# Kernel tuning notes

Hardware: AMD Instinct MI355X
Metric: run time of the kernel (lower is better)

The kernel has to match this reference:

```python
import jax, jax.numpy as jnp
import numpy as np
import math

NBITS = (1, 2, 4, 8)
S, B, D, H, F = 1024, 8, 1024, 16, 4096
HD = D // H


def _quant(w, nbit):
    """Symmetric uniform weight quantization to `nbit` bits with STE."""
    if nbit == 1:
        q = jnp.sign(w) * jnp.mean(jnp.abs(w))
    else:
        qmax = float(2 ** (nbit - 1) - 1)
        scale = jnp.max(jnp.abs(w)) / qmax
        q = jnp.clip(jnp.round(w / scale), -qmax - 1.0, qmax) * scale
    # straight-through estimator: forward uses q, backward flows through w
    return w + jax.lax.stop_gradient(q - w)


def _layernorm(x, g, b, eps=1e-5):
    m = jnp.mean(x, axis=-1, keepdims=True)
    v = jnp.var(x, axis=-1, keepdims=True)
    return (x - m) * jax.lax.rsqrt(v + eps) * g + b


def _quant_attn(src, w_in, b_in, w_out, b_out, nbit):
    # src: [S,B,D]; w_in: [3D,D]; w_out: [D,D]
    w_in_q = _quant(w_in, nbit)
    w_out_q = _quant(w_out, nbit)
    qkv = jnp.einsum('sbd,ed->sbe', src, w_in_q) + b_in  # [S,B,3D]
    q, k, v = jnp.split(qkv, 3, axis=-1)
    q = q.reshape(S, B, H, HD)
    k = k.reshape(S, B, H, HD)
    v = v.reshape(S, B, H, HD)
    scores = jnp.einsum('sbhd,tbhd->bhst', q, k) * (1.0 / math.sqrt(HD))
    p = jax.nn.softmax(scores, axis=-1)  # [B,H,S,S]
    o = jnp.einsum('bhst,tbhd->sbhd', p, v).reshape(S, B, D)
    return jnp.einsum('sbd,ed->sbe', o, w_out_q) + b_out


def setup_inputs() -> dict:
    key = jax.random.key(0)
    ks = jax.random.split(key, 12)
    sc = 0.02
    return {
        'src': jax.random.normal(ks[0], (S, B, D), jnp.float32),
        'alpha': jax.random.normal(ks[1], (3, 4), jnp.float32),
        'in_proj_w': jax.random.normal(ks[2], (4, 3 * D, D), jnp.float32) * sc,
        'in_proj_b': jnp.zeros((4, 3 * D), jnp.float32),
        'out_proj_w': jax.random.normal(ks[3], (4, D, D), jnp.float32) * sc,
        'out_proj_b': jnp.zeros((4, D), jnp.float32),
        'w1': jax.random.normal(ks[4], (4, F, D), jnp.float32) * sc,
        'b1': jnp.zeros((4, F), jnp.float32),
        'w2': jax.random.normal(ks[5], (4, D, F), jnp.float32) * sc,
        'b2': jnp.zeros((4, D), jnp.float32),
        'g1': jnp.ones((D,), jnp.float32),
        'be1': jnp.zeros((D,), jnp.float32),
        'g2': jnp.ones((D,), jnp.float32),
        'be2': jnp.zeros((D,), jnp.float32),
    }


def reference(src, alpha, in_proj_w, in_proj_b, out_proj_w, out_proj_b,
              w1, b1, w2, b2, g1, be1, g2, be2):
    probs = jax.nn.softmax(alpha, axis=-1)  # [3,4]
    # softmax-weighted mixture of multi-bitwidth attention branches
    src2 = jnp.zeros_like(src)
    for i, nbit in enumerate(NBITS):
        src2 = src2 + probs[0, i] * _quant_attn(
            src, in_proj_w[i], in_proj_b[i], out_proj_w[i], out_proj_b[i], nbit)
    x = _layernorm(src + src2, g1, be1)
    # mixture of quantized linear1 branches, then GELU
    h = jnp.zeros((S, B, F), src.dtype)
    for i, nbit in enumerate(NBITS):
        h = h + probs[1, i] * (jnp.einsum('sbd,fd->sbf', x, _quant(w1[i], nbit)) + b1[i])
    h = jax.nn.gelu(h, approximate=False)
    # mixture of quantized linear2 branches
    y = jnp.zeros_like(x)
    for i, nbit in enumerate(NBITS):
        y = y + probs[2, i] * (jnp.einsum('sbf,df->sbd', h, _quant(w2[i], nbit)) + b2[i])
    return _layernorm(x + y, g2, be2)
```

## Files before the change

### kernel.cpp

```cpp
#include <hip/hip_runtime.h>
#include <hip/hip_bf16.h>

typedef __attribute__((ext_vector_type(8))) unsigned short u16x8;
typedef __attribute__((ext_vector_type(4))) unsigned short u16x4;
typedef __attribute__((ext_vector_type(4))) int            i32x4;
typedef __attribute__((ext_vector_type(8))) __bf16         bf16x8;
typedef __attribute__((ext_vector_type(4))) float          f32x4;

#define SS 1024
#define BB 8
#define DD 1024
#define HH 16
#define HDD 64
#define FF 4096
#define MM 8192

#define GL16(g, l) __builtin_amdgcn_global_load_lds( \
    (__attribute__((address_space(1))) const void*)(g), \
    (__attribute__((address_space(3))) void*)(l), 16, 0, 0)

__device__ __forceinline__ float bf2f(unsigned short u) {
    return __uint_as_float(((unsigned int)u) << 16);
}
__device__ __forceinline__ unsigned short f2bf(float f) {
    return __builtin_bit_cast(unsigned short, (__bf16)f);
}
__device__ __forceinline__ float quantv(float w, float som, float qm) {
    if (qm == 0.f) {
        float sgn = (w > 0.f) ? 1.f : ((w < 0.f) ? -1.f : 0.f);
        return sgn * som;
    }
    if (som == 0.f) return 0.f;
    float q = rintf(w / som);
    q = fminf(fmaxf(q, -qm - 1.f), qm);
    return q * som;
}

__global__ __launch_bounds__(256) void k_stats(const float* __restrict__ w_in, const float* __restrict__ w_out,
                                               const float* __restrict__ w1, const float* __restrict__ w2,
                                               const float* __restrict__ src,
                                               float* __restrict__ pmax, float* __restrict__ psum) {
    const int t = blockIdx.y, blk = blockIdx.x, tid = threadIdx.x;
    const float* base; int n;
    if (t < 4)       { base = w_in  + (size_t)t * 3145728;     n = 3145728; }
    else if (t < 8)  { base = w_out + (size_t)(t-4) * 1048576; n = 1048576; }
    else if (t < 12) { base = w1    + (size_t)(t-8) * 4194304; n = 4194304; }
    else if (t < 16) { base = w2    + (size_t)(t-12) * 4194304; n = 4194304; }
    else             { base = src;                             n = 8388608; }
    const int n4 = n >> 2;
    float vmax = 0.f, vsum = 0.f;
    for (int i = blk * 256 + tid; i < n4; i += 65536) {
        float4 v = reinterpret_cast<const float4*>(base)[i];
        float a0 = fabsf(v.x), a1 = fabsf(v.y), a2 = fabsf(v.z), a3 = fabsf(v.w);
        vmax = fmaxf(vmax, fmaxf(fmaxf(a0, a1), fmaxf(a2, a3)));
        vsum += (a0 + a1) + (a2 + a3);
    }
#pragma unroll
    for (int m = 1; m < 64; m <<= 1) { vmax = fmaxf(vmax, __shfl_xor(vmax, m, 64)); vsum += __shfl_xor(vsum, m, 64); }
    __shared__ float sm[4], su[4];
    const int wave = tid >> 6, lane = tid & 63;
    if (lane == 0) { sm[wave] = vmax; su[wave] = vsum; }
    __syncthreads();
    if (tid == 0) {
        pmax[t * 256 + blk] = fmaxf(fmaxf(sm[0], sm[1]), fmaxf(sm[2], sm[3]));
        psum[t * 256 + blk] = (su[0] + su[1]) + (su[2] + su[3]);
    }
}

__global__ __launch_bounds__(256) void k_params(const float* __restrict__ pmax, const float* __restrict__ psum,
                                                const float* __restrict__ alpha, float* __restrict__ P) {
    __shared__ float rm[256], rs[256];
    const int tid = threadIdx.x;
    for (int t = 0; t < 17; ++t) {
        rm[tid] = pmax[t * 256 + tid];
        rs[tid] = psum[t * 256 + tid];
        __syncthreads();
        for (int s = 128; s > 0; s >>= 1) {
            if (tid < s) { rm[tid] = fmaxf(rm[tid], rm[tid + s]); rs[tid] += rs[tid + s]; }
            __syncthreads();
        }
        if (tid == 0) {
            if (t == 16) {
                P[50] = rm[0] * (1.f / 127.f);
            } else {
                const int nbits[4] = {1, 2, 4, 8};
                const int nb = nbits[t & 3];
                float nsize = (t < 4) ? 3145728.f : ((t < 8) ? 1048576.f : 4194304.f);
                if (nb == 1) { P[16 + 2*t] = rs[0] / nsize; P[17 + 2*t] = 0.f; }
                else { float qm = (float)((1 << (nb - 1)) - 1); P[16 + 2*t] = rm[0] / qm; P[17 + 2*t] = qm; }
            }
        }
        __syncthreads();
    }
    if (tid < 3) {
        float a[4], mx = -1e30f;
#pragma unroll
        for (int i = 0; i < 4; ++i) { a[i] = alpha[tid * 4 + i]; mx = fmaxf(mx, a[i]); }
        float e[4], ssum = 0.f;
#pragma unroll
        for (int i = 0; i < 4; ++i) { e[i] = expf(a[i] - mx); ssum += e[i]; }
#pragma unroll
        for (int i = 0; i < 4; ++i) P[tid * 4 + i] = e[i] / ssum;
    }
}

__global__ __launch_bounds__(256) void k_rmax(const float* __restrict__ part, int n, float* __restrict__ out) {
    const int tid = threadIdx.x;
    float m = 0.f;
    for (int i = tid; i < n; i += 256) m = fmaxf(m, part[i]);
#pragma unroll
    for (int s = 1; s < 64; s <<= 1) m = fmaxf(m, __shfl_xor(m, s, 64));
    __shared__ float sm[4];
    const int wave = tid >> 6, lane = tid & 63;
    if (lane == 0) sm[wave] = m;
    __syncthreads();
    if (tid == 0) *out = fmaxf(fmaxf(sm[0], sm[1]), fmaxf(sm[2], sm[3]));
}

__global__ __launch_bounds__(256) void k_quant8(const float* __restrict__ w, signed char* __restrict__ out,
                                                const float* __restrict__ P, int per_tensor, int tbase, int ntot) {
    int i = blockIdx.x * 256 + threadIdx.x;
    if (i >= ntot) return;
    int t = tbase + i / per_tensor;
    float som = P[16 + 2*t], qm = P[17 + 2*t];
    float v;
    float x = w[i];
    if (qm == 0.f)      v = (x > 0.f) ? 1.f : ((x < 0.f) ? -1.f : 0.f);
    else if (som == 0.f) v = 0.f;
    else                v = fminf(fmaxf(rintf(x / som), -qm - 1.f), qm);
    out[i] = (signed char)(int)v;
}

__global__ __launch_bounds__(256) void k_si8(const float* __restrict__ in, signed char* __restrict__ out,
                                             const float* __restrict__ P, int n4) {
    int i = blockIdx.x * 256 + threadIdx.x;
    if (i >= n4) return;
    const float sa = P[50];
    const float inv = (sa > 0.f) ? 1.f / sa : 0.f;
    float4 v = reinterpret_cast<const float4*>(in)[i];
    char4 o;
    o.x = (signed char)(int)fminf(fmaxf(rintf(v.x * inv), -127.f), 127.f);
    o.y = (signed char)(int)fminf(fmaxf(rintf(v.y * inv), -127.f), 127.f);
    o.z = (signed char)(int)fminf(fmaxf(rintf(v.z * inv), -127.f), 127.f);
    o.w = (signed char)(int)fminf(fmaxf(rintf(v.w * inv), -127.f), 127.f);
    reinterpret_cast<char4*>(out)[i] = o;
}

template <int NE, int MODE>
__global__ __launch_bounds__(256) void k_mixq8(const float* __restrict__ w, signed char* __restrict__ out,
                                               float* __restrict__ sB, const float* __restrict__ P,
                                               int tbase, int prow, size_t sz) {
    const int row = blockIdx.x, tid = threadIdx.x;
    const int L = NE * 256;
    float v[NE];
    float lm = 0.f;
#pragma unroll
    for (int j = 0; j < NE; ++j) {
        int k = j * 256 + tid;
        float acc;
        if (MODE == 0) {
            acc = 0.f;
#pragma unroll
            for (int br = 0; br < 4; ++br) {
                int t = tbase + br;
                acc += P[prow * 4 + br] * quantv(w[(size_t)br * sz + (size_t)row * L + k], P[16 + 2*t], P[17 + 2*t]);
            }
        } else {
            int i = k >> 10, e = k & 1023;
            int t = tbase + i;
            acc = P[i] * quantv(w[(size_t)i * sz + (size_t)row * 1024 + e], P[16 + 2*t], P[17 + 2*t]);
        }
        v[j] = acc;
        lm = fmaxf(lm, fabsf(acc));
    }
#pragma unroll
    for (int m = 1; m < 64; m <<= 1) lm = fmaxf(lm, __shfl_xor(lm, m, 64));
    __shared__ float sm[4];
    const int wave = tid >> 6, lane = tid & 63;
    if (lane == 0) sm[wave] = lm;
    __syncthreads();
    lm = fmaxf(fmaxf(sm[0], sm[1]), fmaxf(sm[2], sm[3]));
    if (tid == 0) sB[row] = lm * (1.f / 127.f);
    const float inv = (lm > 0.f) ? 127.f / lm : 0.f;
#pragma unroll
    for (int j = 0; j < NE; ++j)
        out[(size_t)row * L + j * 256 + tid] =
            (signed char)(int)fminf(fmaxf(rintf(v[j] * inv), -127.f), 127.f);
}

__global__ __launch_bounds__(256) void k_mixb(const float* __restrict__ b, float* __restrict__ out,
                                              const float* __restrict__ P, int prow, int n) {
    int i = blockIdx.x * 256 + threadIdx.x;
    if (i >= n) return;
    float acc = 0.f;
#pragma unroll
    for (int br = 0; br < 4; ++br) acc += P[prow * 4 + br] * b[(size_t)br * n + i];
    out[i] = acc;
}

__global__ __launch_bounds__(256) void k_q8(const unsigned short* __restrict__ in, signed char* __restrict__ out,
                                            const float* __restrict__ amax, int n8) {
    int i = blockIdx.x * 256 + threadIdx.x;
    if (i >= n8) return;
    const float am = *amax;
    const float inv = (am > 0.f) ? 127.f / am : 0.f;
    u16x8 v = reinterpret_cast<const u16x8*>(in)[i];
    union { signed char c[8]; unsigned long long u; } r;
#pragma unroll
    for (int e = 0; e < 8; ++e) {
        float f = bf2f(v[e]) * inv;
        r.c[e] = (signed char)(int)fminf(fmaxf(rintf(f), -127.f), 127.f);
    }
    reinterpret_cast<unsigned long long*>(out)[i] = r.u;
}

__global__ __launch_bounds__(256) void k_gemm_i8(const signed char* __restrict__ A,
                                                 const signed char* __restrict__ Bw,
                                                 unsigned short* __restrict__ C,
                                                 const float* __restrict__ bias,
                                                 const float* __restrict__ P, int tIdx,
                                                 int M, int N, int K, int XM, int XN) {
    const int gx = gridDim.x, gy = gridDim.y;
    const int flat = blockIdx.x + gx * blockIdx.y;
    const int xcd = flat & 7, r = flat >> 3;
    const int nloc = gx / XN, mloc = gy / XM;
    const int cm = xcd / XN, cn = xcd - cm * XN;
    const int by = cm * mloc + r / nloc;
    const int bx = cn * nloc + (r - (r / nloc) * nloc);

    __shared__ signed char As[2][128 * 128];
    __shared__ signed char Bs[2][128 * 128];
    const int tid = threadIdx.x;
    const int m0 = by * 128, n0 = bx * 128;
    const int lane = tid & 63, wave = tid >> 6;
    const int wr = wave >> 1, wc = wave & 1;
    const int lr = lane & 15, lg = lane >> 4;
    const int rsub = lane >> 3;
    const int csub = ((lane & 7) ^ rsub) * 16;
    const size_t aoff = (size_t)(m0 + rsub) * K + csub;
    const size_t boff = (size_t)(n0 + rsub) * K + csub;

    i32x4 acc[4][4];
#pragma unroll
    for (int m = 0; m < 4; ++m)
#pragma unroll
        for (int n = 0; n < 4; ++n) acc[m][n] = (i32x4){0, 0, 0, 0};

    auto stage = [&](int buf, int k0) {
#pragma unroll
        for (int it = 0; it < 4; ++it) {
            const int g = it * 4 + wave;
            GL16(A + aoff + (size_t)g * 8 * K + k0, &As[buf][g * 1024]);
            GL16(Bw + boff + (size_t)g * 8 * K + k0, &Bs[buf][g * 1024]);
        }
    };
    auto compute = [&](int buf) {
#pragma unroll
        for (int kh = 0; kh < 2; ++kh) {
            i32x4 af[4], bfr[4];
#pragma unroll
            for (int m = 0; m < 4; ++m) {
                int row = wr * 64 + m * 16 + lr;
                int cidx = (kh * 4 + lg) ^ (lr & 7);
                af[m] = *reinterpret_cast<const i32x4*>(&As[buf][row * 128 + cidx * 16]);
            }
#pragma unroll
            for (int n = 0; n < 4; ++n) {
                int row = wc * 64 + n * 16 + lr;
                int cidx = (kh * 4 + lg) ^ (lr & 7);
                bfr[n] = *reinterpret_cast<const i32x4*>(&Bs[buf][row * 128 + cidx * 16]);
            }
#pragma unroll
            for (int m = 0; m < 4; ++m)
#pragma unroll
                for (int n = 0; n < 4; ++n)
                    acc[m][n] = __builtin_amdgcn_mfma_i32_16x16x64_i8(
                        af[m], bfr[n], acc[m][n], 0, 0, 0);
        }
    };

    stage(0, 0);
    __syncthreads();
    int cur = 0;
    for (int k0 = 128; k0 < K; k0 += 128) {
        stage(cur ^ 1, k0);
        compute(cur);
        __syncthreads();
        cur ^= 1;
    }
    compute(cur);

    const float sab = P[50] * P[16 + 2 * tIdx];
#pragma unroll
    for (int n = 0; n < 4; ++n) {
        const int col = n0 + wc * 64 + n * 16 + lr;
        const float bv = bias[col];
#pragma unroll
        for (int m = 0; m < 4; ++m) {
#pragma unroll
            for (int j = 0; j < 4; ++j) {
                const int row = m0 + wr * 64 + m * 16 + lg * 4 + j;
                float v = (float)acc[m][n][j] * sab + bv;
                C[(size_t)row * N + col] = f2bf(v);
            }
        }
    }
}

__device__ __forceinline__ void store_out(float* C, size_t idx, float v) { C[idx] = v; }
__device__ __forceinline__ void store_out(unsigned short* C, size_t idx, float v) { C[idx] = f2bf(v); }

template <typename OutT, bool GELU>
__global__ __launch_bounds__(256) void k_gemm_i8s(const signed char* __restrict__ A,
                                                  const signed char* __restrict__ Bw,
                                                  OutT* __restrict__ C,
                                                  const float* __restrict__ bias,
                                                  const float* __restrict__ sB,
                                                  const float* __restrict__ aAm,
                                                  float* __restrict__ oPart,
                                                  int M, int N, int K, int XM, int XN) {
    const int gx = gridDim.x, gy = gridDim.y;
    const int flat = blockIdx.x + gx * blockIdx.y;
    const int xcd = flat & 7, r = flat >> 3;
    const int nloc = gx / XN, mloc = gy / XM;
    const int cm = xcd / XN, cn = xcd - cm * XN;
    const int by = cm * mloc + r / nloc;
    const int bx = cn * nloc + (r - (r / nloc) * nloc);

    __shared__ signed char As[2][128 * 128];
    __shared__ signed char Bs[2][128 * 128];
    __shared__ float smx[4];
    const int tid = threadIdx.x;
    const int m0 = by * 128, n0 = bx * 128;
    const int lane = tid & 63, wave = tid >> 6;
    const int wr = wave >> 1, wc = wave & 1;
    const int lr = lane & 15, lg = lane >> 4;
    const int rsub = lane >> 3;
    const int csub = ((lane & 7) ^ rsub) * 16;
    const size_t aoff = (size_t)(m0 + rsub) * K + csub;
    const size_t boff = (size_t)(n0 + rsub) * K + csub;

    i32x4 acc[4][4];
#pragma unroll
    for (int m = 0; m < 4; ++m)
#pragma unroll
        for (int n = 0; n < 4; ++n) acc[m][n] = (i32x4){0, 0, 0, 0};

    auto stage = [&](int buf, int k0) {
#pragma unroll
        for (int it = 0; it < 4; ++it) {
            const int g = it * 4 + wave;
            GL16(A + aoff + (size_t)g * 8 * K + k0, &As[buf][g * 1024]);
            GL16(Bw + boff + (size_t)g * 8 * K + k0, &Bs[buf][g * 1024]);
        }
    };
    auto compute = [&](int buf) {
#pragma unroll
        for (int kh = 0; kh < 2; ++kh) {
            i32x4 af[4], bfr[4];
#pragma unroll
            for (int m = 0; m < 4; ++m) {
                int row = wr * 64 + m * 16 + lr;
                int cidx = (kh * 4 + lg) ^ (lr & 7);
                af[m] = *reinterpret_cast<const i32x4*>(&As[buf][row * 128 + cidx * 16]);
            }
#pragma unroll
            for (int n = 0; n < 4; ++n) {
                int row = wc * 64 + n * 16 + lr;
                int cidx = (kh * 4 + lg) ^ (lr & 7);
                bfr[n] = *reinterpret_cast<const i32x4*>(&Bs[buf][row * 128 + cidx * 16]);
            }
#pragma unroll
            for (int m = 0; m < 4; ++m)
#pragma unroll
                for (int n = 0; n < 4; ++n)
                    acc[m][n] = __builtin_amdgcn_mfma_i32_16x16x64_i8(
                        af[m], bfr[n], acc[m][n], 0, 0, 0);
        }
    };

    stage(0, 0);
    __syncthreads();
    int cur = 0;
    for (int k0 = 128; k0 < K; k0 += 128) {
        stage(cur ^ 1, k0);
        compute(cur);
        __syncthreads();
        cur ^= 1;
    }
    compute(cur);

    const float sA = (*aAm) * (1.f / 127.f);
    float lm = 0.f;
#pragma unroll
    for (int n = 0; n < 4; ++n) {
        const int col = n0 + wc * 64 + n * 16 + lr;
        const float sc = sA * sB[col];
        const float bv = bias ? bias[col] : 0.f;
#pragma unroll
        for (int m = 0; m < 4; ++m) {
#pragma unroll
            for (int j = 0; j < 4; ++j) {
                const int row = m0 + wr * 64 + m * 16 + lg * 4 + j;
                float v = (float)acc[m][n][j] * sc + bv;
                if (GELU) v = 0.5f * v * (1.f + erff(v * 0.70710678118654752f));
                store_out(C, (size_t)row * N + col, v);
                if (oPart) lm = fmaxf(lm, fabsf(v));
            }
        }
    }
    if (oPart) {
#pragma unroll
        for (int m = 1; m < 64; m <<= 1) lm = fmaxf(lm, __shfl_xor(lm, m, 64));
        if (lane == 0) smx[wave] = lm;
        __syncthreads();
        if (tid == 0) oPart[flat] = fmaxf(fmaxf(smx[0], smx[1]), fmaxf(smx[2], smx[3]));
    }
}

__global__ __launch_bounds__(256) void k_fmfma(const unsigned short* __restrict__ qkvb, int qstride,
                                               unsigned short* __restrict__ outb, int ostride,
                                               float* __restrict__ oPart) {
    __shared__ unsigned short Ks[64 * 64];
    __shared__ unsigned short Vt[64 * 64];
    __shared__ unsigned short Pl[4 * 16 * 72];
    __shared__ float smx[4];
    const int tid = threadIdx.x;
    const int lane = tid & 63, wave = tid >> 6;
    const int lr = lane & 15, lg = lane >> 4;
    const int f = blockIdx.x;
    const int bh = (f & 7) * 16 + (f >> 7);
    const int s0 = ((f >> 3) & 15) * 64;
    const int b = bh >> 4, hh = bh & 15;
    const int hb = hh * 64;

    u16x8 qf[2];
    {
        const size_t qb = (size_t)((s0 + wave * 16 + lr) * 8 + b) * qstride + hb;
#pragma unroll
        for (int ks = 0; ks < 2; ++ks)
            qf[ks] = *reinterpret_cast<const u16x8*>(qkvb + qb + ks * 32 + lg * 8);
    }
    const int rsub = lane >> 3;
    const int csub = ((lane & 7) ^ rsub) * 8;
    const unsigned short* kS = qkvb + (size_t)(rsub * 8 + b) * qstride + 1024 + hb + csub;

    float m_old = -1e30f, l_run = 0.f;
    f32x4 oacc[4];
#pragma unroll
    for (int n = 0; n < 4; ++n) oacc[n] = (f32x4){0.f, 0.f, 0.f, 0.f};
    unsigned short* myP = Pl + wave * (16 * 72);

    for (int kt = 0; kt < 16; ++kt) {
        __syncthreads();
#pragma unroll
        for (int it = 0; it < 2; ++it) {
            const int g = it * 4 + wave;
            GL16(kS + (size_t)((kt * 64 + g * 8) * 8) * qstride, &Ks[g * 512]);
        }
#pragma unroll
        for (int it = 0; it < 2; ++it) {
            int c = tid + it * 256;
            int row = c >> 3, ch = c & 7;
            const size_t gb = (size_t)((kt * 64 + row) * 8 + b) * qstride + hb + ch * 8;
            u16x8 vv = *reinterpret_cast<const u16x8*>(qkvb + gb + 2048);
            const int vbase = ((row >> 3) ^ ch) * 8 + (row & 7);
#pragma unroll
            for (int e = 0; e < 8; ++e) Vt[(ch * 8 + e) * 64 + (vbase ^ (e * 8))] = vv[e];
        }
        __syncthreads();
        f32x4 sacc[4];
#pragma unroll
        for (int n = 0; n < 4; ++n) sacc[n] = (f32x4){0.f, 0.f, 0.f, 0.f};
#pragma unroll
        for (int ks = 0; ks < 2; ++ks) {
#pragma unroll
            for (int n = 0; n < 4; ++n) {
                int row = n * 16 + lr;
                int cidx = (ks * 4 + lg) ^ (lr & 7);
                u16x8 kf = *reinterpret_cast<const u16x8*>(&Ks[row * 64 + cidx * 8]);
                sacc[n] = __builtin_amdgcn_mfma_f32_16x16x32_bf16(
                    __builtin_bit_cast(bf16x8, kf), __builtin_bit_cast(bf16x8, qf[ks]),
                    sacc[n], 0, 0, 0);
            }
        }
        float pmax = -1e30f;
#pragma unroll
        for (int n = 0; n < 4; ++n)
#pragma unroll
            for (int j = 0; j < 4; ++j) { sacc[n][j] *= 0.125f; pmax = fmaxf(pmax, sacc[n][j]); }
        pmax = fmaxf(pmax, __shfl_xor(pmax, 16, 64));
        pmax = fmaxf(pmax, __shfl_xor(pmax, 32, 64));
        const float m_new = fmaxf(m_old, pmax);
        const float corr = __expf(m_old - m_new);
        float pv[16];
        float psum = 0.f;
#pragma unroll
        for (int n = 0; n < 4; ++n)
#pragma unroll
            for (int j = 0; j < 4; ++j) { float e = __expf(sacc[n][j] - m_new); pv[n * 4 + j] = e; psum += e; }
        psum += __shfl_xor(psum, 16, 64);
        psum += __shfl_xor(psum, 32, 64);
        l_run = l_run * corr + psum;
        m_old = m_new;
#pragma unroll
        for (int n = 0; n < 4; ++n)
#pragma unroll
            for (int t2 = 0; t2 < 2; ++t2) {
                int key = n * 16 + lg * 4 + t2 * 2;
                unsigned int pk =
                    (unsigned int)__builtin_bit_cast(unsigned short, (__bf16)pv[n * 4 + t2 * 2]) |
                    ((unsigned int)__builtin_bit_cast(unsigned short, (__bf16)pv[n * 4 + t2 * 2 + 1]) << 16);
                *reinterpret_cast<unsigned int*>(&myP[lr * 72 + key]) = pk;
            }
#pragma unroll
        for (int j = 0; j < 4; ++j) {
            float cj = __shfl(corr, lg * 4 + j, 64);
#pragma unroll
            for (int n = 0; n < 4; ++n) oacc[n][j] *= cj;
        }
#pragma unroll
        for (int ks = 0; ks < 2; ++ks) {
            u16x8 pa = *reinterpret_cast<const u16x8*>(&myP[lr * 72 + ks * 32 + lg * 8]);
#pragma unroll
            for (int n = 0; n < 4; ++n) {
                int d = n * 16 + lr;
                int kcs = ((ks * 4 + lg) ^ (d >> 3)) ^ (d & 7);
                u16x8 vf = *reinterpret_cast<const u16x8*>(&Vt[d * 64 + kcs * 8]);
                oacc[n] = __builtin_amdgcn_mfma_f32_16x16x32_bf16(
                    __builtin_bit_cast(bf16x8, pa), __builtin_bit_cast(bf16x8, vf),
                    oacc[n], 0, 0, 0);
            }
        }
    }
    const float linv = 1.f / l_run;
    float lm = 0.f;
#pragma unroll
    for (int j = 0; j < 4; ++j) {
        float lj = __shfl(linv, lg * 4 + j, 64);
        const size_t rowb = (size_t)((s0 + wave * 16 + lg * 4 + j) * 8 + b) * ostride + hb;
#pragma unroll
        for (int n = 0; n < 4; ++n) {
            float v = oacc[n][j] * lj;
            outb[rowb + n * 16 + lr] = f2bf(v);
            lm = fmaxf(lm, fabsf(v));
        }
    }
#pragma unroll
    for (int m = 1; m < 64; m <<= 1) lm = fmaxf(lm, __shfl_xor(lm, m, 64));
    if (lane == 0) smx[wave] = lm;
    __syncthreads();
    if (tid == 0) oPart[f] = fmaxf(fmaxf(smx[0], smx[1]), fmaxf(smx[2], smx[3]));
}

__global__ __launch_bounds__(256) void k_ln(const float* __restrict__ xf, const unsigned short* __restrict__ xb,
                                            const float* __restrict__ r,
                                            const float* __restrict__ g, const float* __restrict__ be,
                                            float* __restrict__ outf, unsigned short* __restrict__ outb,
                                            float* __restrict__ oPart) {
    const int row = blockIdx.x, tid = threadIdx.x;
    const size_t base = (size_t)row * 1024 + tid * 4;
    float x0, x1, x2, x3;
    if (xf) {
        float4 xv = *reinterpret_cast<const float4*>(xf + base);
        x0 = xv.x; x1 = xv.y; x2 = xv.z; x3 = xv.w;
    } else {
        u16x4 xv = *reinterpret_cast<const u16x4*>(xb + base);
        x0 = bf2f(xv[0]); x1 = bf2f(xv[1]); x2 = bf2f(xv[2]); x3 = bf2f(xv[3]);
    }
    float4 rv = *reinterpret_cast<const float4*>(r + base);
    float t0 = x0 + rv.x, t1 = x1 + rv.y, t2 = x2 + rv.z, t3 = x3 + rv.w;
    float s = t0 + t1 + t2 + t3;
    float ss = t0 * t0 + t1 * t1 + t2 * t2 + t3 * t3;
#pragma unroll
    for (int m = 1; m < 64; m <<= 1) { s += __shfl_xor(s, m, 64); ss += __shfl_xor(ss, m, 64); }
    __shared__ float red[8];
    __shared__ float smx[4];
    const int wave = tid >> 6, lane = tid & 63;
    if (lane == 0) { red[wave] = s; red[4 + wave] = ss; }
    __syncthreads();
    s = red[0] + red[1] + red[2] + red[3];
    ss = red[4] + red[5] + red[6] + red[7];
    const float mean = s * (1.f / 1024.f);
    const float var = ss * (1.f / 1024.f) - mean * mean;
    const float rstd = rsqrtf(var + 1e-5f);
    float4 gv = *reinterpret_cast<const float4*>(g + tid * 4);
    float4 bv = *reinterpret_cast<const float4*>(be + tid * 4);
    float o0 = (t0 - mean) * rstd * gv.x + bv.x;
    float o1 = (t1 - mean) * rstd * gv.y + bv.y;
    float o2 = (t2 - mean) * rstd * gv.z + bv.z;
    float o3 = (t3 - mean) * rstd * gv.w + bv.w;
    if (outf) {
        float4 ov = {o0, o1, o2, o3};
        *reinterpret_cast<float4*>(outf + base) = ov;
    }
    if (outb) {
        u16x4 q; q[0] = f2bf(o0); q[1] = f2bf(o1); q[2] = f2bf(o2); q[3] = f2bf(o3);
        *reinterpret_cast<u16x4*>(outb + base) = q;
    }
    if (oPart) {
        float lm = fmaxf(fmaxf(fabsf(o0), fabsf(o1)), fmaxf(fabsf(o2), fabsf(o3)));
#pragma unroll
        for (int m = 1; m < 64; m <<= 1) lm = fmaxf(lm, __shfl_xor(lm, m, 64));
        if (lane == 0) smx[wave] = lm;
        __syncthreads();
        if (tid == 0) oPart[row] = fmaxf(fmaxf(smx[0], smx[1]), fmaxf(smx[2], smx[3]));
    }
}

extern "C" void kernel_launch(void* const* d_in, const int* in_sizes, int n_in,
                              void* d_out, int out_size, void* d_ws, size_t ws_size,
                              hipStream_t stream) {
    const float* src   = (const float*)d_in[0];
    const float* alpha = (const float*)d_in[1];
    const float* w_in  = (const float*)d_in[2];
    const float* b_in  = (const float*)d_in[3];
    const float* w_out = (const float*)d_in[4];
    const float* b_out = (const float*)d_in[5];
    const float* w1    = (const float*)d_in[6];
    const float* b1    = (const float*)d_in[7];
    const float* w2    = (const float*)d_in[8];
    const float* b2    = (const float*)d_in[9];
    const float* g1    = (const float*)d_in[10];
    const float* be1   = (const float*)d_in[11];
    const float* g2    = (const float*)d_in[12];
    const float* be2   = (const float*)d_in[13];

    char* ws = (char*)d_ws;
    size_t off = 0;
    auto alloc = [&](size_t bytes) { size_t r = off; off += (bytes + 255) & ~(size_t)255; return r; };
    float* P              = (float*)(ws + alloc(1024));
    float* amaxv          = (float*)(ws + alloc(256));
    float* flashPart      = (float*)(ws + alloc(8192 * 4));
    float* lnPart         = (float*)(ws + alloc(8192 * 4));
    float* hPart          = (float*)(ws + alloc(2048 * 4));
    float* pmax           = (float*)(ws + alloc(17 * 256 * 4));
    float* psum           = (float*)(ws + alloc(17 * 256 * 4));
    signed char* WinQ8    = (signed char*)(ws + alloc((size_t)4 * 3072 * 1024));
    signed char* WoutC8   = (signed char*)(ws + alloc((size_t)1024 * 4096));
    float* sOut           = (float*)(ws + alloc(1024 * 4));
    signed char* W1m8     = (signed char*)(ws + alloc((size_t)4096 * 1024));
    float* s1             = (float*)(ws + alloc(4096 * 4));
    signed char* W2m8     = (signed char*)(ws + alloc((size_t)1024 * 4096));
    float* s2             = (float*)(ws + alloc(1024 * 4));
    float* b1m            = (float*)(ws + alloc(4096 * 4));
    float* b2m            = (float*)(ws + alloc(1024 * 4));
    float* bOm            = (float*)(ws + alloc(1024 * 4));
    signed char* Si8      = (signed char*)(ws + alloc((size_t)MM * 1024));
    unsigned short* Xbf   = (unsigned short*)(ws + alloc((size_t)MM * 1024 * 2));
    signed char* Xi8      = (signed char*)(ws + alloc((size_t)MM * 1024));
    unsigned short* attnC = (unsigned short*)(ws + alloc((size_t)MM * 4096 * 2));
    unsigned short* qkvB  = (unsigned short*)(ws + alloc((size_t)MM * 3072 * 2));
    signed char* attnC8   = (signed char*)qkvB;
    unsigned short* h     = attnC;
    signed char* h8       = (signed char*)qkvB;
    if (ws_size < off) return;

    float* outF = (float*)d_out;

    k_stats<<<dim3(256, 17), 256, 0, stream>>>(w_in, w_out, w1, w2, src, pmax, psum);
    k_params<<<1, 256, 0, stream>>>(pmax, psum, alpha, P);
    {
        int n = 4 * 3072 * 1024;
        k_quant8<<<(n + 255) / 256, 256, 0, stream>>>(w_in, WinQ8, P, 3072 * 1024, 0, n);
        k_mixq8<16, 1><<<1024, 256, 0, stream>>>(w_out, WoutC8, sOut, P, 4, 0, 1048576);
        k_mixq8<4, 0><<<4096, 256, 0, stream>>>(w1, W1m8, s1, P, 8, 1, 4194304);
        k_mixq8<16, 0><<<1024, 256, 0, stream>>>(w2, W2m8, s2, P, 12, 2, 4194304);
        k_mixb<<<(4096 + 255) / 256, 256, 0, stream>>>(b1, b1m, P, 1, 4096);
        k_mixb<<<(1024 + 255) / 256, 256, 0, stream>>>(b2, b2m, P, 2, 1024);
        k_mixb<<<(1024 + 255) / 256, 256, 0, stream>>>(b_out, bOm, P, 0, 1024);
        k_si8<<<(2097152 + 255) / 256, 256, 0, stream>>>(src, Si8, P, 2097152);
    }
    for (int i = 0; i < 4; ++i) {
        k_gemm_i8<<<dim3(24, 64), 256, 0, stream>>>(
            Si8, WinQ8 + (size_t)i * 3072 * 1024, qkvB, b_in + i * 3072, P, i, MM, 3072, 1024, 1, 8);
        k_fmfma<<<dim3(2048), 256, 0, stream>>>(qkvB, 3072, attnC + i * 1024, 4096,
                                                flashPart + i * 2048);
    }
    k_rmax<<<1, 256, 0, stream>>>(flashPart, 8192, amaxv + 0);
    k_q8<<<(4194304 + 255) / 256, 256, 0, stream>>>(attnC, attnC8, amaxv + 0, 4194304);
    k_gemm_i8s<float, false><<<dim3(8, 64), 256, 0, stream>>>(
        attnC8, WoutC8, outF, bOm, sOut, amaxv + 0, nullptr, MM, 1024, 4096, 4, 2);
    k_ln<<<MM, 256, 0, stream>>>(src, nullptr, outF, g1, be1, nullptr, Xbf, lnPart);
    k_rmax<<<1, 256, 0, stream>>>(lnPart, 8192, amaxv + 1);
    k_q8<<<(1048576 + 255) / 256, 256, 0, stream>>>(Xbf, Xi8, amaxv + 1, 1048576);
    k_gemm_i8s<unsigned short, true><<<dim3(32, 64), 256, 0, stream>>>(
        Xi8, W1m8, h, b1m, s1, amaxv + 1, hPart, MM, 4096, 1024, 1, 8);
    k_rmax<<<1, 256, 0, stream>>>(hPart, 2048, amaxv + 2);
    k_q8<<<(4194304 + 255) / 256, 256, 0, stream>>>(h, h8, amaxv + 2, 4194304);
    k_gemm_i8s<float, false><<<dim3(8, 64), 256, 0, stream>>>(
        h8, W2m8, outF, b2m, s2, amaxv + 2, nullptr, MM, 1024, 4096, 4, 2);
    k_ln<<<MM, 256, 0, stream>>>(nullptr, Xbf, outF, g2, be2, outF, nullptr, nullptr);
}
```

Baseline: 934.8 us.

## Double-buffer K/V tiles and process two query subtiles per wave in flash attention

The flash-attention kernel now uses 512-thread blocks covering 256 query rows each, and each wave handles two 16-row query subtiles. This reuses every staged K/V tile across more queries. K and V tiles are double-buffered so the next tile's loads are issued before computing on the current one, leaving one barrier per iteration. The row-sum reduction is deferred to the end. The grid shrinks to a quarter of its previous size, which may reduce parallelism, and LDS and register use rise.

```diff
diff --git a/kernel.cpp b/kernel.cpp
--- a/kernel.cpp
+++ b/kernel.cpp
@@ -418,139 +418,154 @@
     }
 }
 
-__global__ __launch_bounds__(256) void k_fmfma(const unsigned short* __restrict__ qkvb, int qstride,
+__global__ __launch_bounds__(512) void k_fmfma(const unsigned short* __restrict__ qkvb, int qstride,
                                                unsigned short* __restrict__ outb, int ostride,
                                                float* __restrict__ oPart) {
-    __shared__ unsigned short Ks[64 * 64];
-    __shared__ unsigned short Vt[64 * 64];
-    __shared__ unsigned short Pl[4 * 16 * 72];
-    __shared__ float smx[4];
+    __shared__ unsigned short Ks[2][4096];
+    __shared__ unsigned short Vt[2][4096];
+    __shared__ unsigned short Pl[8 * 16 * 72];
+    __shared__ float smx[8];
     const int tid = threadIdx.x;
     const int lane = tid & 63, wave = tid >> 6;
     const int lr = lane & 15, lg = lane >> 4;
     const int f = blockIdx.x;
-    const int bh = (f & 7) * 16 + (f >> 7);
-    const int s0 = ((f >> 3) & 15) * 64;
+    const int bh = (f & 7) * 16 + ((f >> 3) & 15);
+    const int s0 = (f >> 7) * 256;
     const int b = bh >> 4, hh = bh & 15;
     const int hb = hh * 64;
 
-    u16x8 qf[2];
-    {
-        const size_t qb = (size_t)((s0 + wave * 16 + lr) * 8 + b) * qstride + hb;
+    u16x8 qf[2][2];
+#pragma unroll
+    for (int qf2 = 0; qf2 < 2; ++qf2) {
+        const size_t qb = (size_t)((s0 + wave * 32 + qf2 * 16 + lr) * 8 + b) * qstride + hb;
 #pragma unroll
         for (int ks = 0; ks < 2; ++ks)
-            qf[ks] = *reinterpret_cast<const u16x8*>(qkvb + qb + ks * 32 + lg * 8);
+            qf[qf2][ks] = *reinterpret_cast<const u16x8*>(qkvb + qb + ks * 32 + lg * 8);
     }
     const int rsub = lane >> 3;
     const int csub = ((lane & 7) ^ rsub) * 8;
     const unsigned short* kS = qkvb + (size_t)(rsub * 8 + b) * qstride + 1024 + hb + csub;
 
-    float m_old = -1e30f, l_run = 0.f;
-    f32x4 oacc[4];
-#pragma unroll
-    for (int n = 0; n < 4; ++n) oacc[n] = (f32x4){0.f, 0.f, 0.f, 0.f};
+    float m_old[2] = {-1e30f, -1e30f};
+    float l_lane[2] = {0.f, 0.f};
+    f32x4 oacc[2][4];
+#pragma unroll
+    for (int qf2 = 0; qf2 < 2; ++qf2)
+#pragma unroll
+        for (int n = 0; n < 4; ++n) oacc[qf2][n] = (f32x4){0.f, 0.f, 0.f, 0.f};
     unsigned short* myP = Pl + wave * (16 * 72);
 
+    auto stage = [&](int buf, int kt) {
+        GL16(kS + (size_t)((kt * 64 + wave * 8) * 8) * qstride, &Ks[buf][wave * 512]);
+        const int row = tid >> 3, ch = tid & 7;
+        const size_t gb = (size_t)((kt * 64 + row) * 8 + b) * qstride + hb + ch * 8;
+        u16x8 vv = *reinterpret_cast<const u16x8*>(qkvb + gb + 2048);
+        const int vbase = ((row >> 3) ^ ch) * 8 + (row & 7);
+#pragma unroll
+        for (int e = 0; e < 8; ++e) Vt[buf][(ch * 8 + e) * 64 + (vbase ^ (e * 8))] = vv[e];
+    };
+
+    stage(0, 0);
+    __syncthreads();
+    int cur = 0;
     for (int kt = 0; kt < 16; ++kt) {
+        if (kt < 15) stage(cur ^ 1, kt + 1);
+#pragma unroll
+        for (int qf2 = 0; qf2 < 2; ++qf2) {
+            f32x4 sacc[4];
+#pragma unroll
+            for (int n = 0; n < 4; ++n) sacc[n] = (f32x4){0.f, 0.f, 0.f, 0.f};
+#pragma unroll
+            for (int ks = 0; ks < 2; ++ks) {
+#pragma unroll
+                for (int n = 0; n < 4; ++n) {
+                    int row = n * 16 + lr;
+                    int cidx = (ks * 4 + lg) ^ (lr & 7);
+                    u16x8 kf = *reinterpret_cast<const u16x8*>(&Ks[cur][row * 64 + cidx * 8]);
+                    sacc[n] = __builtin_amdgcn_mfma_f32_16x16x32_bf16(
+                        __builtin_bit_cast(bf16x8, kf), __builtin_bit_cast(bf16x8, qf[qf2][ks]),
+                        sacc[n], 0, 0, 0);
+                }
+            }
+            float pmax = -1e30f;
+#pragma unroll
+            for (int n = 0; n < 4; ++n)
+#pragma unroll
+                for (int j = 0; j < 4; ++j) { sacc[n][j] *= 0.125f; pmax = fmaxf(pmax, sacc[n][j]); }
+            pmax = fmaxf(pmax, __shfl_xor(pmax, 16, 64));
+            pmax = fmaxf(pmax, __shfl_xor(pmax, 32, 64));
+            const float m_new = fmaxf(m_old[qf2], pmax);
+            const float corr = __expf(m_old[qf2] - m_new);
+            float pv[16];
+            float psum = 0.f;
+#pragma unroll
+            for (int n = 0; n < 4; ++n)
+#pragma unroll
+                for (int j = 0; j < 4; ++j) { float e = __expf(sacc[n][j] - m_new); pv[n * 4 + j] = e; psum += e; }
+            l_lane[qf2] = l_lane[qf2] * corr + psum;
+            m_old[qf2] = m_new;
+#pragma unroll
+            for (int n = 0; n < 4; ++n)
+#pragma unroll
+                for (int t2 = 0; t2 < 2; ++t2) {
+                    int key = n * 16 + lg * 4 + t2 * 2;
+                    unsigned int pk =
+                        (unsigned int)__builtin_bit_cast(unsigned short, (__bf16)pv[n * 4 + t2 * 2]) |
+                        ((unsigned int)__builtin_bit_cast(unsigned short, (__bf16)pv[n * 4 + t2 * 2 + 1]) << 16);
+                    *reinterpret_cast<unsigned int*>(&myP[lr * 72 + key]) = pk;
+                }
+#pragma unroll
+            for (int j = 0; j < 4; ++j) {
+                float cj = __shfl(corr, lg * 4 + j, 64);
+#pragma unroll
+                for (int n = 0; n < 4; ++n) oacc[qf2][n][j] *= cj;
+            }
+#pragma unroll
+            for (int ks = 0; ks < 2; ++ks) {
+                u16x8 pa = *reinterpret_cast<const u16x8*>(&myP[lr * 72 + ks * 32 + lg * 8]);
+#pragma unroll
+                for (int n = 0; n < 4; ++n) {
+                    int d = n * 16 + lr;
+                    int kcs = ((ks * 4 + lg) ^ (d >> 3)) ^ (d & 7);
+                    u16x8 vf = *reinterpret_cast<const u16x8*>(&Vt[cur][d * 64 + kcs * 8]);
+                    oacc[qf2][n] = __builtin_amdgcn_mfma_f32_16x16x32_bf16(
+                        __builtin_bit_cast(bf16x8, pa), __builtin_bit_cast(bf16x8, vf),
+                        oacc[qf2][n], 0, 0, 0);
+                }
+            }
+        }
         __syncthreads();
-#pragma unroll
-        for (int it = 0; it < 2; ++it) {
-            const int g = it * 4 + wave;
-            GL16(kS + (size_t)((kt * 64 + g * 8) * 8) * qstride, &Ks[g * 512]);
-        }
-#pragma unroll
-        for (int it = 0; it < 2; ++it) {
-            int c = tid + it * 256;
-            int row = c >> 3, ch = c & 7;
-            const size_t gb = (size_t)((kt * 64 + row) * 8 + b) * qstride + hb + ch * 8;
-            u16x8 vv = *reinterpret_cast<const u16x8*>(qkvb + gb + 2048);
-            const int vbase = ((row >> 3) ^ ch) * 8 + (row & 7);
-#pragma unroll
-            for (int e = 0; e < 8; ++e) Vt[(ch * 8 + e) * 64 + (vbase ^ (e * 8))] = vv[e];
-        }
-        __syncthreads();
-        f32x4 sacc[4];
-#pragma unroll
-        for (int n = 0; n < 4; ++n) sacc[n] = (f32x4){0.f, 0.f, 0.f, 0.f};
-#pragma unroll
-        for (int ks = 0; ks < 2; ++ks) {
+        cur ^= 1;
+    }
+    float lm = 0.f;
+#pragma unroll
+    for (int qf2 = 0; qf2 < 2; ++qf2) {
+        float lsum = l_lane[qf2];
+        lsum += __shfl_xor(lsum, 16, 64);
+        lsum += __shfl_xor(lsum, 32, 64);
+        const float linv = 1.f / lsum;
+#pragma unroll
+        for (int j = 0; j < 4; ++j) {
+            float lj = __shfl(linv, lg * 4 + j, 64);
+            const size_t rowb = (size_t)((s0 + wave * 32 + qf2 * 16 + lg * 4 + j) * 8 + b) * ostride + hb;
 #pragma unroll
             for (int n = 0; n < 4; ++n) {
-                int row = n * 16 + lr;
-                int cidx = (ks * 4 + lg) ^ (lr & 7);
-                u16x8 kf = *reinterpret_cast<const u16x8*>(&Ks[row * 64 + cidx * 8]);
-                sacc[n] = __builtin_amdgcn_mfma_f32_16x16x32_bf16(
-                    __builtin_bit_cast(bf16x8, kf), __builtin_bit_cast(bf16x8, qf[ks]),
-                    sacc[n], 0, 0, 0);
-            }
-        }
-        float pmax = -1e30f;
-#pragma unroll
-        for (int n = 0; n < 4; ++n)
-#pragma unroll
-            for (int j = 0; j < 4; ++j) { sacc[n][j] *= 0.125f; pmax = fmaxf(pmax, sacc[n][j]); }
-        pmax = fmaxf(pmax, __shfl_xor(pmax, 16, 64));
-        pmax = fmaxf(pmax, __shfl_xor(pmax, 32, 64));
-        const float m_new = fmaxf(m_old, pmax);
-        const float corr = __expf(m_old - m_new);
-        float pv[16];
-        float psum = 0.f;
-#pragma unroll
-        for (int n = 0; n < 4; ++n)
-#pragma unroll
-            for (int j = 0; j < 4; ++j) { float e = __expf(sacc[n][j] - m_new); pv[n * 4 + j] = e; psum += e; }
-        psum += __shfl_xor(psum, 16, 64);
-        psum += __shfl_xor(psum, 32, 64);
-        l_run = l_run * corr + psum;
-        m_old = m_new;
-#pragma unroll
-        for (int n = 0; n < 4; ++n)
-#pragma unroll
-            for (int t2 = 0; t2 < 2; ++t2) {
-                int key = n * 16 + lg * 4 + t2 * 2;
-                unsigned int pk =
-                    (unsigned int)__builtin_bit_cast(unsigned short, (__bf16)pv[n * 4 + t2 * 2]) |
-                    ((unsigned int)__builtin_bit_cast(unsigned short, (__bf16)pv[n * 4 + t2 * 2 + 1]) << 16);
-                *reinterpret_cast<unsigned int*>(&myP[lr * 72 + key]) = pk;
-            }
-#pragma unroll
-        for (int j = 0; j < 4; ++j) {
-            float cj = __shfl(corr, lg * 4 + j, 64);
-#pragma unroll
-            for (int n = 0; n < 4; ++n) oacc[n][j] *= cj;
-        }
-#pragma unroll
-        for (int ks = 0; ks < 2; ++ks) {
-            u16x8 pa = *reinterpret_cast<const u16x8*>(&myP[lr * 72 + ks * 32 + lg * 8]);
-#pragma unroll
-            for (int n = 0; n < 4; ++n) {
-                int d = n * 16 + lr;
-                int kcs = ((ks * 4 + lg) ^ (d >> 3)) ^ (d & 7);
-                u16x8 vf = *reinterpret_cast<const u16x8*>(&Vt[d * 64 + kcs * 8]);
-                oacc[n] = __builtin_amdgcn_mfma_f32_16x16x32_bf16(
-                    __builtin_bit_cast(bf16x8, pa), __builtin_bit_cast(bf16x8, vf),
-                    oacc[n], 0, 0, 0);
-            }
-        }
-    }
-    const float linv = 1.f / l_run;
-    float lm = 0.f;
-#pragma unroll
-    for (int j = 0; j < 4; ++j) {
-        float lj = __shfl(linv, lg * 4 + j, 64);
-        const size_t rowb = (size_t)((s0 + wave * 16 + lg * 4 + j) * 8 + b) * ostride + hb;
-#pragma unroll
-        for (int n = 0; n < 4; ++n) {
-            float v = oacc[n][j] * lj;
-            outb[rowb + n * 16 + lr] = f2bf(v);
-            lm = fmaxf(lm, fabsf(v));
+                float v = oacc[qf2][n][j] * lj;
+                outb[rowb + n * 16 + lr] = f2bf(v);
+                lm = fmaxf(lm, fabsf(v));
+            }
         }
     }
 #pragma unroll
     for (int m = 1; m < 64; m <<= 1) lm = fmaxf(lm, __shfl_xor(lm, m, 64));
     if (lane == 0) smx[wave] = lm;
     __syncthreads();
-    if (tid == 0) oPart[f] = fmaxf(fmaxf(smx[0], smx[1]), fmaxf(smx[2], smx[3]));
+    if (tid == 0) {
+        float t = 0.f;
+#pragma unroll
+        for (int w = 0; w < 8; ++w) t = fmaxf(t, smx[w]);
+        oPart[f] = t;
+    }
 }
 
 __global__ __launch_bounds__(256) void k_ln(const float* __restrict__ xf, const unsigned short* __restrict__ xb,
@@ -674,10 +689,10 @@
     for (int i = 0; i < 4; ++i) {
         k_gemm_i8<<<dim3(24, 64), 256, 0, stream>>>(
             Si8, WinQ8 + (size_t)i * 3072 * 1024, qkvB, b_in + i * 3072, P, i, MM, 3072, 1024, 1, 8);
-        k_fmfma<<<dim3(2048), 256, 0, stream>>>(qkvB, 3072, attnC + i * 1024, 4096,
-                                                flashPart + i * 2048);
-    }
-    k_rmax<<<1, 256, 0, stream>>>(flashPart, 8192, amaxv + 0);
+        k_fmfma<<<dim3(512), 512, 0, stream>>>(qkvB, 3072, attnC + i * 1024, 4096,
+                                               flashPart + i * 512);
+    }
+    k_rmax<<<1, 256, 0, stream>>>(flashPart, 2048, amaxv + 0);
     k_q8<<<(4194304 + 255) / 256, 256, 0, stream>>>(attnC, attnC8, amaxv + 0, 4194304);
     k_gemm_i8s<float, false><<<dim3(8, 64), 256, 0, stream>>>(
         attnC8, WoutC8, outF, bOm, sOut, amaxv + 0, nullptr, MM, 1024, 4096, 4, 2);
```

Measured after the change: 935.2 us. Within noise of the previous version (+0.0%).
